# Optimization experiments

Hardware: AMD Instinct MI355X
Metric: run time of the kernel (lower is better)

Reference implementation:

```python
import jax, jax.numpy as jnp
import numpy as np

N_HEADS = 16
EPS = 1e-6

def _split_heads(x, h):
    b, t, d = x.shape
    return x.reshape(b, t, h, d // h).transpose(0, 2, 1, 3)  # b h t e

def _elu_fm(x):
    # elu(x) + 1, the default feature map
    return jax.nn.elu(x) + 1.0

def setup_inputs() -> dict:
    key = jax.random.key(0)
    kq, kk, kv = jax.random.split(key, 3)
    shape = (4, 4096, 1024)
    return {
        "query": jax.random.normal(kq, shape, dtype=jnp.float32),
        "key": jax.random.normal(kk, shape, dtype=jnp.float32),
        "value": jax.random.normal(kv, shape, dtype=jnp.float32),
    }

def reference(query, key, value):
    q = _split_heads(query, N_HEADS)   # b h t e
    k = _split_heads(key, N_HEADS)     # b h s e
    v = _split_heads(value, N_HEADS)   # b h s d
    Q = _elu_fm(q)
    K = _elu_fm(k)
    # non-causal linear attention (attn_mask=None path)
    k_sum = K.sum(axis=-2)                                   # b h e
    D_inv = 1.0 / (jnp.einsum('bhne,bhe->bhn', Q, k_sum) + EPS)
    context = jnp.einsum('bhse,bhsd->bhed', K, v)            # b h e d
    out = jnp.einsum('bhed,bhne,bhn->bhnd', context, Q, D_inv)
    b, h, t, d = out.shape
    return out.transpose(0, 2, 1, 3).reshape(b, t, h * d)    # b t (h d)
```

## Files before the change

kernel.cpp:

```cpp
#include <hip/hip_runtime.h>
#include <cmath>

#define T_SEQ 4096
#define D_MODEL 1024
#define EPS 1e-6f
#define CHUNKS 16

typedef __attribute__((ext_vector_type(8))) short bf16x8;
typedef __attribute__((ext_vector_type(4))) float f32x4;

__device__ __forceinline__ float elu1(float x) { return x > 0.f ? x + 1.f : __expf(x); }

__device__ __forceinline__ unsigned f2bf_u(float f) {
    union { float f; unsigned u; } v; v.f = f;
    unsigned r = v.u + 0x7fffu + ((v.u >> 16) & 1u);
    return r >> 16;
}
__device__ __forceinline__ short f2bf(float f) { return (short)f2bf_u(f); }
__device__ __forceinline__ unsigned packbf(float lo, float hi) {
    return f2bf_u(lo) | (f2bf_u(hi) << 16);
}
__device__ __forceinline__ unsigned cvt_pk_bf16(float lo, float hi) {
    unsigned r;
    asm("v_cvt_pk_bf16_f32 %0, %1, %2" : "=v"(r) : "v"(lo), "v"(hi));
    return r;
}
__device__ __forceinline__ int swz(int e) { return ((e >> 2) ^ (e >> 4)) & 3; }

__global__ __launch_bounds__(1024) void ctx_fused(const float* __restrict__ K,
                                                  const float* __restrict__ V,
                                                  float* __restrict__ partial) {
    __shared__ __align__(16) short sT[2][4][2][64 * 40];

    const int bb = blockIdx.x >> 6;
    const int hq = (blockIdx.x >> 4) & 3;
    const int ch = blockIdx.x & 15;
    const int tid = threadIdx.x;
    const int wave = tid >> 6, lane = tid & 63;
    const int hh = wave >> 2, qd = wave & 3, eh = qd >> 1, dh = qd & 1;
    const int g = lane >> 4, r = lane & 15;
    const int u = wave, c6 = lane;
    const int hw = c6 >> 4;
    const int eq = c6 & 15;

    const size_t base = (size_t)bb * T_SEQ * D_MODEL;
    const int s0 = ch * 256;
    const int colb = hq * 256;

    f32x4 acc[2][2], accs[2];
#pragma unroll
    for (int i = 0; i < 2; ++i)
#pragma unroll
        for (int q = 0; q < 4; ++q) { accs[i][q] = 0.f; acc[i][0][q] = 0.f; acc[i][1][q] = 0.f; }

    bf16x8 ones;
    const short ob = (r == 0) ? (short)0x3F80 : (short)0;
#pragma unroll
    for (int j = 0; j < 8; ++j) ones[j] = ob;

    float4 kf[2], vf[2];
    auto load_tile = [&](int kt) {
        const float* Kp = K + base + (size_t)(s0 + 32 * kt + 2 * u) * D_MODEL + colb + 4 * c6;
        const float* Vp = V + base + (size_t)(s0 + 32 * kt + 2 * u) * D_MODEL + colb + 4 * c6;
        kf[0] = *(const float4*)Kp;
        kf[1] = *(const float4*)(Kp + D_MODEL);
        vf[0] = *(const float4*)Vp;
        vf[1] = *(const float4*)(Vp + D_MODEL);
    };
    auto store_tile = [&](int buf) {
        short* tk = &sT[buf][hw][0][0];
        short* tv = &sT[buf][hw][1][0];
        const float* k0 = (const float*)&kf[0];
        const float* k1 = (const float*)&kf[1];
        const float* v0 = (const float*)&vf[0];
        const float* v1 = (const float*)&vf[1];
        const int sl2 = 2 * ((u & 3) ^ (hw & 3));
#pragma unroll
        for (int i = 0; i < 4; ++i) {
            const int e = 4 * eq + i;
            const int off = e * 40 + 8 * ((u >> 2) ^ swz(e) ^ (hw & 3)) + sl2;
            *(unsigned*)&tk[off] = packbf(elu1(k0[i]), elu1(k1[i]));
            *(unsigned*)&tv[off] = packbf(v0[i], v1[i]);
        }
    };
    auto compute = [&](int buf) {
        const short* tk = &sT[buf][hh][0][0];
        const short* tv = &sT[buf][hh][1][0];
        const int h3 = hh & 3;
        bf16x8 a[2], bv[2];
#pragma unroll
        for (int mi = 0; mi < 2; ++mi) {
            const int e = 32 * eh + 16 * mi + r;
            a[mi] = *(const bf16x8*)&tk[e * 40 + 8 * (g ^ swz(e) ^ h3)];
        }
#pragma unroll
        for (int ni = 0; ni < 2; ++ni) {
            const int d = 32 * dh + 16 * ni + r;
            bv[ni] = *(const bf16x8*)&tv[d * 40 + 8 * (g ^ swz(d) ^ h3)];
        }
#pragma unroll
        for (int mi = 0; mi < 2; ++mi) {
#pragma unroll
            for (int ni = 0; ni < 2; ++ni)
                acc[mi][ni] = __builtin_amdgcn_mfma_f32_16x16x32_bf16(a[mi], bv[ni], acc[mi][ni], 0, 0, 0);
            if (dh == 0)
                accs[mi] = __builtin_amdgcn_mfma_f32_16x16x32_bf16(a[mi], ones, accs[mi], 0, 0, 0);
        }
    };

    load_tile(0);
    store_tile(0);
    __syncthreads();
#pragma unroll 1
    for (int t = 0; t < 8; ++t) {
        if (t < 7) load_tile(t + 1);
        compute(t & 1);
        if (t < 7) store_tile((t + 1) & 1);
        __syncthreads();
    }

    float* slab = partial + ((size_t)((bb * 16 + hq * 4 + hh) * CHUNKS + ch)) * 4160;
#pragma unroll
    for (int mi = 0; mi < 2; ++mi)
#pragma unroll
        for (int ni = 0; ni < 2; ++ni)
            *(f32x4*)&slab[qd * 1024 + (mi * 2 + ni) * 256 + lane * 4] = acc[mi][ni];
    if (dh == 0 && r == 0) {
#pragma unroll
        for (int mi = 0; mi < 2; ++mi)
#pragma unroll
            for (int q = 0; q < 4; ++q)
                slab[4096 + 32 * eh + 16 * mi + 4 * g + q] = accs[mi][q];
    }
}

__global__ __launch_bounds__(256) void ctx_reduce(const float* __restrict__ partial,
                                                  ushort* __restrict__ ctxbf) {
    const int head = blockIdx.x >> 2, part = blockIdx.x & 3;
    const float* pbase = partial + (size_t)head * CHUNKS * 4160;
    ushort* cbase = ctxbf + (size_t)head * 4160;
    const int lo = part * 260;
    for (int i4 = lo + threadIdx.x; i4 < lo + 260; i4 += 256) {
        f32x4 s;
#pragma unroll
        for (int k = 0; k < 4; ++k) s[k] = 0.f;
#pragma unroll
        for (int c = 0; c < CHUNKS; ++c) {
            const f32x4 v = *(const f32x4*)&pbase[(size_t)c * 4160 + i4 * 4];
#pragma unroll
            for (int k = 0; k < 4; ++k) s[k] += v[k];
        }
        const int f0 = i4 * 4;
        if (f0 < 4096) {
#pragma unroll
            for (int k = 0; k < 4; ++k) {
                const int f = f0 + k;
                const int qd = f >> 10, t2 = (f >> 8) & 3, ln = (f >> 2) & 63, q = f & 3;
                const int e = 32 * (qd >> 1) + 16 * (t2 >> 1) + 4 * (ln >> 4) + q;
                const int d = 32 * (qd & 1) + 16 * (t2 & 1) + (ln & 15);
                cbase[d * 64 + e] = (ushort)f2bf(s[k]);
            }
        } else {
#pragma unroll
            for (int k = 0; k < 4; ++k) cbase[f0 + k] = (ushort)f2bf(s[k]);
        }
    }
}

__global__ __launch_bounds__(256, 4) void attn_out(const float* __restrict__ Q,
                                                   const ushort* __restrict__ ctxbf,
                                                   float* __restrict__ out) {
    const int head = blockIdx.x >> 4, nb = blockIdx.x & 15;
    const int b = head >> 4, h = head & 15;
    const int tid = threadIdx.x, wave = tid >> 6, lane = tid & 63;
    const int g = lane >> 4, r = lane & 15;
    const ushort* C = ctxbf + (size_t)head * 4160;

    bf16x8 bfr[2][5];
#pragma unroll
    for (int kt = 0; kt < 2; ++kt) {
#pragma unroll
        for (int n = 0; n < 4; ++n)
            bfr[kt][n] = *(const bf16x8*)&C[(16 * n + r) * 64 + kt * 32 + 8 * g];
        bf16x8 ks = *(const bf16x8*)&C[4096 + kt * 32 + 8 * g];
        if (r != 0) {
#pragma unroll
            for (int j = 0; j < 8; ++j) ks[j] = 0;
        }
        bfr[kt][4] = ks;
    }

    const int n0 = nb * 256 + wave * 64;
    const float* qbase = Q + ((size_t)b * T_SEQ + n0) * D_MODEL + (size_t)h * 64;

    f32x4 acc[4][5];
#pragma unroll
    for (int m = 0; m < 4; ++m)
#pragma unroll
        for (int n = 0; n < 5; ++n)
#pragma unroll
            for (int q = 0; q < 4; ++q) acc[m][n][q] = 0.f;

    union U8 { unsigned u[4]; bf16x8 v; };
#pragma unroll
    for (int kt = 0; kt < 2; ++kt)
#pragma unroll
        for (int m = 0; m < 4; ++m) {
            const float* qp = qbase + (size_t)(16 * m + r) * D_MODEL + kt * 32 + 8 * g;
            const float4 q1 = *(const float4*)qp;
            const float4 q2 = *(const float4*)(qp + 4);
            U8 a;
            a.u[0] = cvt_pk_bf16(elu1(q1.x), elu1(q1.y));
            a.u[1] = cvt_pk_bf16(elu1(q1.z), elu1(q1.w));
            a.u[2] = cvt_pk_bf16(elu1(q2.x), elu1(q2.y));
            a.u[3] = cvt_pk_bf16(elu1(q2.z), elu1(q2.w));
#pragma unroll
            for (int n = 0; n < 5; ++n)
                acc[m][n] = __builtin_amdgcn_mfma_f32_16x16x32_bf16(a.v, bfr[kt][n], acc[m][n], 0, 0, 0);
        }

#pragma unroll
    for (int m = 0; m < 4; ++m) {
        float dinv[4];
#pragma unroll
        for (int q = 0; q < 4; ++q)
            dinv[q] = 1.f / (__shfl(acc[m][4][q], lane & 48) + EPS);
#pragma unroll
        for (int q = 0; q < 4; ++q) {
            float* op = out + ((size_t)b * T_SEQ + n0 + 16 * m + 4 * g + q) * D_MODEL
                        + (size_t)h * 64 + r;
#pragma unroll
            for (int n = 0; n < 4; ++n) op[16 * n] = acc[m][n][q] * dinv[q];
        }
    }
}

extern "C" void kernel_launch(void* const* d_in, const int* in_sizes, int n_in,
                              void* d_out, int out_size, void* d_ws, size_t ws_size,
                              hipStream_t stream) {
    const float* Q = (const float*)d_in[0];
    const float* K = (const float*)d_in[1];
    const float* V = (const float*)d_in[2];
    float* out = (float*)d_out;

    float* partial  = out;
    ushort* ctxbf   = (ushort*)d_ws;

    hipLaunchKernelGGL(ctx_fused,  dim3(256),  dim3(1024), 0, stream, K, V, partial);
    hipLaunchKernelGGL(ctx_reduce, dim3(256),  dim3(256),  0, stream, partial, ctxbf);
    hipLaunchKernelGGL(attn_out,   dim3(1024), dim3(256),  0, stream, Q, ctxbf, out);
}
```

Baseline: 58.44 us.

## Deepen global-load prefetch to three tiles ahead with register ring buffer

The K/V tile loads now run three iterations ahead, held in a four-slot register ring, so more global memory latency is hidden behind MFMA compute. The main loop is fully unrolled so slot indices become compile-time constants. __syncthreads is replaced by an explicit lgkmcnt wait plus s_barrier with sched_barriers, which avoids waiting on outstanding vector memory loads at each barrier. The deeper prefetch raises register pressure and could lower occupancy.

Result: no change. 58.03 us (-0.7%).

```diff
diff --git a/kernel.cpp b/kernel.cpp
--- a/kernel.cpp
+++ b/kernel.cpp
@@ -58,22 +58,22 @@
 #pragma unroll
     for (int j = 0; j < 8; ++j) ones[j] = ob;
 
-    float4 kf[2], vf[2];
-    auto load_tile = [&](int kt) {
+    float4 kf[4][2], vf[4][2];
+    auto load_tile = [&](int kt, int slot) {
         const float* Kp = K + base + (size_t)(s0 + 32 * kt + 2 * u) * D_MODEL + colb + 4 * c6;
         const float* Vp = V + base + (size_t)(s0 + 32 * kt + 2 * u) * D_MODEL + colb + 4 * c6;
-        kf[0] = *(const float4*)Kp;
-        kf[1] = *(const float4*)(Kp + D_MODEL);
-        vf[0] = *(const float4*)Vp;
-        vf[1] = *(const float4*)(Vp + D_MODEL);
+        kf[slot][0] = *(const float4*)Kp;
+        kf[slot][1] = *(const float4*)(Kp + D_MODEL);
+        vf[slot][0] = *(const float4*)Vp;
+        vf[slot][1] = *(const float4*)(Vp + D_MODEL);
     };
-    auto store_tile = [&](int buf) {
+    auto store_tile = [&](int buf, int slot) {
         short* tk = &sT[buf][hw][0][0];
         short* tv = &sT[buf][hw][1][0];
-        const float* k0 = (const float*)&kf[0];
-        const float* k1 = (const float*)&kf[1];
-        const float* v0 = (const float*)&vf[0];
-        const float* v1 = (const float*)&vf[1];
+        const float* k0 = (const float*)&kf[slot][0];
+        const float* k1 = (const float*)&kf[slot][1];
+        const float* v0 = (const float*)&vf[slot][0];
+        const float* v1 = (const float*)&vf[slot][1];
         const int sl2 = 2 * ((u & 3) ^ (hw & 3));
 #pragma unroll
         for (int i = 0; i < 4; ++i) {
@@ -108,15 +108,23 @@
         }
     };
 
-    load_tile(0);
-    store_tile(0);
-    __syncthreads();
-#pragma unroll 1
+    load_tile(0, 0);
+    load_tile(1, 1);
+    load_tile(2, 2);
+    store_tile(0, 0);
+    asm volatile("s_waitcnt lgkmcnt(0)" ::: "memory");
+    __builtin_amdgcn_s_barrier();
+    __builtin_amdgcn_sched_barrier(0);
+
+#pragma unroll
     for (int t = 0; t < 8; ++t) {
-        if (t < 7) load_tile(t + 1);
+        if (t + 3 < 8) load_tile(t + 3, (t + 3) & 3);
         compute(t & 1);
-        if (t < 7) store_tile((t + 1) & 1);
-        __syncthreads();
+        if (t + 1 < 8) store_tile((t + 1) & 1, (t + 1) & 3);
+        __builtin_amdgcn_sched_barrier(0);
+        asm volatile("s_waitcnt lgkmcnt(0)" ::: "memory");
+        __builtin_amdgcn_s_barrier();
+        __builtin_amdgcn_sched_barrier(0);
     }
 
     float* slab = partial + ((size_t)((bb * 16 + hq * 4 + hh) * CHUNKS + ch)) * 4160;
```

## Stage K/V tiles via direct global-to-LDS loads and convert in compute

Applied to the files above, without the earlier changes.

Replaces the register-staged load, ELU, bf16 pack and swizzled LDS store with `__builtin_amdgcn_global_load_lds` copies of raw fp32 K/V rows into a padded LDS buffer (row stride 257). Each wave then reads its MFMA fragments column-wise as scalar floats, applies ELU+1 and packs to bf16 with `v_cvt_pk_bf16_f32` before the MFMAs. The aim is to drop the VGPR round trip and the store phase, and to let the next tile's loads overlap compute asynchronously. In exchange, LDS use roughly doubles because tiles are stored as fp32. There are many more scalar LDS reads per fragment, and ELU/convert work is repeated across waves that share the same K columns. Rows are only 4-byte aligned for the 16-byte LDS DMA.

Measured after the change: 57.90 us. No clear change (-0.9%).

```diff
diff --git a/kernel.cpp b/kernel.cpp
--- a/kernel.cpp
+++ b/kernel.cpp
@@ -5,6 +5,7 @@
 #define D_MODEL 1024
 #define EPS 1e-6f
 #define CHUNKS 16
+#define RSTRIDE 257
 
 typedef __attribute__((ext_vector_type(8))) short bf16x8;
 typedef __attribute__((ext_vector_type(4))) float f32x4;
@@ -17,20 +18,16 @@
     return r >> 16;
 }
 __device__ __forceinline__ short f2bf(float f) { return (short)f2bf_u(f); }
-__device__ __forceinline__ unsigned packbf(float lo, float hi) {
-    return f2bf_u(lo) | (f2bf_u(hi) << 16);
-}
 __device__ __forceinline__ unsigned cvt_pk_bf16(float lo, float hi) {
     unsigned r;
     asm("v_cvt_pk_bf16_f32 %0, %1, %2" : "=v"(r) : "v"(lo), "v"(hi));
     return r;
 }
-__device__ __forceinline__ int swz(int e) { return ((e >> 2) ^ (e >> 4)) & 3; }
 
 __global__ __launch_bounds__(1024) void ctx_fused(const float* __restrict__ K,
                                                   const float* __restrict__ V,
                                                   float* __restrict__ partial) {
-    __shared__ __align__(16) short sT[2][4][2][64 * 40];
+    __shared__ __align__(16) float sL[2][2][32 * RSTRIDE];
 
     const int bb = blockIdx.x >> 6;
     const int hq = (blockIdx.x >> 4) & 3;
@@ -39,9 +36,7 @@
     const int wave = tid >> 6, lane = tid & 63;
     const int hh = wave >> 2, qd = wave & 3, eh = qd >> 1, dh = qd & 1;
     const int g = lane >> 4, r = lane & 15;
-    const int u = wave, c6 = lane;
-    const int hw = c6 >> 4;
-    const int eq = c6 & 15;
+    const int u = wave;
 
     const size_t base = (size_t)bb * T_SEQ * D_MODEL;
     const int s0 = ch * 256;
@@ -58,45 +53,52 @@
 #pragma unroll
     for (int j = 0; j < 8; ++j) ones[j] = ob;
 
-    float4 kf[2], vf[2];
-    auto load_tile = [&](int kt) {
-        const float* Kp = K + base + (size_t)(s0 + 32 * kt + 2 * u) * D_MODEL + colb + 4 * c6;
-        const float* Vp = V + base + (size_t)(s0 + 32 * kt + 2 * u) * D_MODEL + colb + 4 * c6;
-        kf[0] = *(const float4*)Kp;
-        kf[1] = *(const float4*)(Kp + D_MODEL);
-        vf[0] = *(const float4*)Vp;
-        vf[1] = *(const float4*)(Vp + D_MODEL);
+    union U8 { unsigned u[4]; bf16x8 v; };
+
+    auto stage = [&](int t, int buf) {
+        const size_t gr = base + (size_t)(s0 + 32 * t + 2 * u) * D_MODEL + colb + 4 * lane;
+        const float* Kp = K + gr;
+        const float* Vp = V + gr;
+        float* dK = &sL[buf][0][(2 * u) * RSTRIDE];
+        float* dV = &sL[buf][1][(2 * u) * RSTRIDE];
+        __builtin_amdgcn_global_load_lds((const unsigned*)Kp, (unsigned*)dK, 16, 0, 0);
+        __builtin_amdgcn_global_load_lds((const unsigned*)(Kp + D_MODEL),
+                                         (unsigned*)(dK + RSTRIDE), 16, 0, 0);
+        __builtin_amdgcn_global_load_lds((const unsigned*)Vp, (unsigned*)dV, 16, 0, 0);
+        __builtin_amdgcn_global_load_lds((const unsigned*)(Vp + D_MODEL),
+                                         (unsigned*)(dV + RSTRIDE), 16, 0, 0);
     };
-    auto store_tile = [&](int buf) {
-        short* tk = &sT[buf][hw][0][0];
-        short* tv = &sT[buf][hw][1][0];
-        const float* k0 = (const float*)&kf[0];
-        const float* k1 = (const float*)&kf[1];
-        const float* v0 = (const float*)&vf[0];
-        const float* v1 = (const float*)&vf[1];
-        const int sl2 = 2 * ((u & 3) ^ (hw & 3));
-#pragma unroll
-        for (int i = 0; i < 4; ++i) {
-            const int e = 4 * eq + i;
-            const int off = e * 40 + 8 * ((u >> 2) ^ swz(e) ^ (hw & 3)) + sl2;
-            *(unsigned*)&tk[off] = packbf(elu1(k0[i]), elu1(k1[i]));
-            *(unsigned*)&tv[off] = packbf(v0[i], v1[i]);
-        }
-    };
+
     auto compute = [&](int buf) {
-        const short* tk = &sT[buf][hh][0][0];
-        const short* tv = &sT[buf][hh][1][0];
-        const int h3 = hh & 3;
+        const float* tk = &sL[buf][0][0];
+        const float* tv = &sL[buf][1][0];
+        const int hb = hh * 64;
         bf16x8 a[2], bv[2];
 #pragma unroll
         for (int mi = 0; mi < 2; ++mi) {
-            const int e = 32 * eh + 16 * mi + r;
-            a[mi] = *(const bf16x8*)&tk[e * 40 + 8 * (g ^ swz(e) ^ h3)];
+            const int col = hb + 32 * eh + 16 * mi + r;
+            float f[8];
+#pragma unroll
+            for (int j = 0; j < 8; ++j) f[j] = tk[(8 * g + j) * RSTRIDE + col];
+            U8 t;
+            t.u[0] = cvt_pk_bf16(elu1(f[0]), elu1(f[1]));
+            t.u[1] = cvt_pk_bf16(elu1(f[2]), elu1(f[3]));
+            t.u[2] = cvt_pk_bf16(elu1(f[4]), elu1(f[5]));
+            t.u[3] = cvt_pk_bf16(elu1(f[6]), elu1(f[7]));
+            a[mi] = t.v;
         }
 #pragma unroll
         for (int ni = 0; ni < 2; ++ni) {
-            const int d = 32 * dh + 16 * ni + r;
-            bv[ni] = *(const bf16x8*)&tv[d * 40 + 8 * (g ^ swz(d) ^ h3)];
+            const int col = hb + 32 * dh + 16 * ni + r;
+            float f[8];
+#pragma unroll
+            for (int j = 0; j < 8; ++j) f[j] = tv[(8 * g + j) * RSTRIDE + col];
+            U8 t;
+            t.u[0] = cvt_pk_bf16(f[0], f[1]);
+            t.u[1] = cvt_pk_bf16(f[2], f[3]);
+            t.u[2] = cvt_pk_bf16(f[4], f[5]);
+            t.u[3] = cvt_pk_bf16(f[6], f[7]);
+            bv[ni] = t.v;
         }
 #pragma unroll
         for (int mi = 0; mi < 2; ++mi) {
@@ -108,14 +110,12 @@
         }
     };
 
-    load_tile(0);
-    store_tile(0);
+    stage(0, 0);
     __syncthreads();
 #pragma unroll 1
     for (int t = 0; t < 8; ++t) {
-        if (t < 7) load_tile(t + 1);
+        if (t < 7) stage(t + 1, (t + 1) & 1);
         compute(t & 1);
-        if (t < 7) store_tile((t + 1) & 1);
         __syncthreads();
     }
 
```
